# Optimization experiments

Hardware: AMD Instinct MI355X
Metric: run time of the kernel (lower is better)

The kernel has to match this reference:

```python
import jax, jax.numpy as jnp
import numpy as np

B, L, D = 32, 512, 512
H = 512            # d_inner
N_LAYERS = 2
K_SCALE = 1.0
M_SCALE = 1.0
MAX_NORM = 10.0
RMS_EPS = 1e-5


def setup_inputs() -> dict:
    key = jax.random.key(0)
    ks = jax.random.split(key, 12)
    s = 0.02
    x = jax.random.normal(ks[0], (B, L, D), dtype=jnp.float32)
    norm_w = jnp.ones((D,), dtype=jnp.float32)
    W_ih = jax.random.normal(ks[1], (N_LAYERS, D, 2 * H), dtype=jnp.float32) * s
    b_ih = jnp.zeros((N_LAYERS, 2 * H), dtype=jnp.float32)
    W_hh = jax.random.normal(ks[2], (N_LAYERS, H, 2 * H), dtype=jnp.float32) * s
    b_hh = jnp.zeros((N_LAYERS, 2 * H), dtype=jnp.float32)
    # base decay lambdas in [0.01, 0.2] (per KOSLMSSM.__init__), stored as log
    lam = np.linspace(0.01, 0.2, H).astype(np.float32)
    log_lambda = jnp.broadcast_to(jnp.log(jnp.asarray(lam)), (N_LAYERS, H))
    k_W1 = jax.random.normal(ks[3], (N_LAYERS, H, 3 * H), dtype=jnp.float32) * s
    k_b1 = jnp.zeros((N_LAYERS, 3 * H), dtype=jnp.float32)
    k_W2 = jax.random.normal(ks[4], (N_LAYERS, 3 * H, H), dtype=jnp.float32) * s
    k_b2 = jnp.zeros((N_LAYERS, H), dtype=jnp.float32)
    Wo = jax.random.normal(ks[5], (N_LAYERS, H, D), dtype=jnp.float32) * s
    return {"x": x, "norm_w": norm_w, "W_ih": W_ih, "b_ih": b_ih,
            "W_hh": W_hh, "b_hh": b_hh, "log_lambda": log_lambda,
            "k_W1": k_W1, "k_b1": k_b1, "k_W2": k_W2, "k_b2": k_b2, "Wo": Wo}


def _rmsnorm(x, w):
    return x * jax.lax.rsqrt(jnp.mean(x * x, axis=-1, keepdims=True) + RMS_EPS) * w


def _layer(x, norm_w, W_ih, b_ih, W_hh, b_hh, log_lambda, k_W1, k_b1, k_W2, k_b2, Wo):
    xn = _rmsnorm(x, norm_w)
    # input-to-gate projection for the whole sequence (one big GEMM)
    gx = jnp.einsum('bld,dg->blg', xn, W_ih) + b_ih          # [B,L,2H]
    A_base = 1.0 - jnp.exp(log_lambda)                        # [H], stable decay

    def step(carry, g_t):
        h, c, A = carry                                       # each [B,H]
        g = g_t + h @ W_hh + b_hh                             # [B,2H]
        z, m = jnp.split(g, 2, axis=-1)                       # z_raw, m_raw
        M = jnp.tanh(m) * M_SCALE
        innov = z - A * c - M                                 # fused innovation
        kmid = jax.nn.gelu(innov @ k_W1 + k_b1, approximate=False)
        K = jnp.tanh(kmid @ k_W2 + k_b2) * (K_SCALE * 0.5)    # gain
        A_new = A_base * (1.0 - K * K)                        # contractive diag
        c_new = A_new * c + K * innov + M
        sumsq = jnp.sum(c_new * c_new, axis=-1, keepdims=True)
        scale = jnp.minimum(1.0, MAX_NORM * jax.lax.rsqrt(sumsq + 1e-6))
        c_new = c_new * scale
        h_new = c_new
        return (h_new, c_new, A_new), h_new

    z0 = jnp.zeros((x.shape[0], H), dtype=x.dtype)
    _, hs = jax.lax.scan(step, (z0, z0, z0), jnp.swapaxes(gx, 0, 1))
    hs = jnp.swapaxes(hs, 0, 1)                               # [B,L,H]
    return jnp.einsum('blh,hd->bld', hs, Wo)


def reference(x, norm_w, W_ih, b_ih, W_hh, b_hh, log_lambda,
              k_W1, k_b1, k_W2, k_b2, Wo):
    for l in range(N_LAYERS):
        x = _layer(x, norm_w, W_ih[l], b_ih[l], W_hh[l], b_hh[l],
                   log_lambda[l], k_W1[l], k_b1[l], k_W2[l], k_b2[l], Wo[l])
    return x
```

## Files before the change

kernel.cpp:

```cpp
#include <hip/hip_runtime.h>
#include <math.h>

#define BB   32
#define LSEQ 512
#define DD   512
#define HH   512
#define G2H  1024
#define K3H  1536

#define NG   8
#define GWG  64
#define FPAD 16

typedef unsigned int u32;
typedef _Float16 half2_t __attribute__((ext_vector_type(2)));
typedef u32 v4u __attribute__((ext_vector_type(4)));

__device__ __forceinline__ void mload4(v4u& d, const u32* p) {
  asm volatile("global_load_dwordx4 %0, %1, off sc1" : "=v"(d) : "v"(p));
}
__device__ __forceinline__ void vmwait4(v4u& a, v4u& b, v4u& c, v4u& d) {
  asm volatile("s_waitcnt vmcnt(0)"
               : "+v"(a), "+v"(b), "+v"(c), "+v"(d) :: "memory");
}
__device__ __forceinline__ void mstore(u32* p, u32 v) {
  asm volatile("global_store_dword %0, %1, off sc0 sc1" :: "v"(p), "v"(v)
               : "memory");
}

__device__ __forceinline__ float dot2acc(u32 a, u32 b, float acc) {
#if __has_builtin(__builtin_amdgcn_fdot2)
  return __builtin_amdgcn_fdot2(__builtin_bit_cast(half2_t, a),
                                __builtin_bit_cast(half2_t, b), acc, false);
#else
  half2_t ha = __builtin_bit_cast(half2_t, a);
  half2_t hb = __builtin_bit_cast(half2_t, b);
  return acc + (float)ha[0] * (float)hb[0] + (float)ha[1] * (float)hb[1];
#endif
}
__device__ __forceinline__ float dotq(v4u a, v4u b, float acc) {
  acc = dot2acc(a.x, b.x, acc);
  acc = dot2acc(a.y, b.y, acc);
  acc = dot2acc(a.z, b.z, acc);
  acc = dot2acc(a.w, b.w, acc);
  return acc;
}
__device__ __forceinline__ u32 pkf16(float a, float b) {
#if __has_builtin(__builtin_amdgcn_cvt_pkrtz)
  return __builtin_bit_cast(u32, __builtin_amdgcn_cvt_pkrtz(a, b));
#else
  half2_t h; h[0] = (_Float16)a; h[1] = (_Float16)b;
  return __builtin_bit_cast(u32, h);
#endif
}

template<int M> struct TreeC {
  static __device__ __forceinline__ void run(float* a, int lane, int d) {
    const bool hi = (lane & d) != 0;
#pragma unroll
    for (int i = 0; i < M / 2; ++i) {
      float mine  = hi ? a[2 * i + 1] : a[2 * i];
      float yours = hi ? a[2 * i]     : a[2 * i + 1];
      a[i] = mine + __shfl_xor(yours, d, 64);
    }
    TreeC<M / 2>::run(a, lane, d << 1);
  }
};
template<> struct TreeC<1> {
  static __device__ __forceinline__ void run(float*, int, int) {}
};
template<int M>
__device__ __forceinline__ float tree_reduce(float* a, int lane) {
  TreeC<M>::run(a, lane, 1);
  float v = a[0];
#pragma unroll
  for (int d = M; d <= 32; d <<= 1) v += __shfl_xor(v, d, 64);
  return v;
}

__device__ __forceinline__ void xbar(u32* arrive, u32* go, int slot,
                                     unsigned gen, int tid) {
  __syncthreads();
  if (slot == 0) {
    if (tid >= 1 && tid < GWG)
      while (__hip_atomic_load(&arrive[tid * FPAD], __ATOMIC_RELAXED,
                               __HIP_MEMORY_SCOPE_AGENT) < gen) {}
    __syncthreads();
    if (tid == 0) mstore(go, gen);
  } else {
    if (tid == 0) {
      mstore(&arrive[slot * FPAD], gen);
      while (__hip_atomic_load(go, __ATOMIC_RELAXED,
                               __HIP_MEMORY_SCOPE_AGENT) < gen) {}
    }
  }
  __syncthreads();
}

__global__ __launch_bounds__(256)
void rmsnorm_kernel(const float* __restrict__ x, const float* __restrict__ w,
                    float* __restrict__ y)
{
  __shared__ float redl[256];
  const long row = blockIdx.x;
  const int t = threadIdx.x;
  const float* xr = x + row * DD;
  float v0 = xr[t], v1 = xr[t + 256];
  redl[t] = v0 * v0 + v1 * v1;
  __syncthreads();
  for (int off = 128; off > 0; off >>= 1) {
    if (t < off) redl[t] += redl[t + off];
    __syncthreads();
  }
  float scale = rsqrtf(redl[0] * (1.0f / 512.0f) + 1e-5f);
  float* yr = y + row * DD;
  yr[t]       = v0 * scale * w[t];
  yr[t + 256] = v1 * scale * w[t + 256];
}

__global__ __launch_bounds__(256)
void gemm_fp32(const float* __restrict__ A, const float* __restrict__ B,
               const float* __restrict__ bias, float* __restrict__ C,
               int M, int N, int K)
{
  __shared__ float As[16][68];
  __shared__ float Bs[16][64];
  const int t  = threadIdx.x;
  const int tx = t & 15, ty = t >> 4;
  const long m0 = (long)blockIdx.x * 64;
  const long n0 = (long)blockIdx.y * 64;
  const int ar = t >> 2, ac = (t & 3) * 4;
  const int bk = t >> 4, bn = (t & 15) * 4;
  float acc[4][4] = {{0.f}};

  for (int k0 = 0; k0 < K; k0 += 16) {
    float4 av = *(const float4*)(A + (m0 + ar) * K + k0 + ac);
    float4 bv = *(const float4*)(B + (long)(k0 + bk) * N + n0 + bn);
    As[ac + 0][ar] = av.x; As[ac + 1][ar] = av.y;
    As[ac + 2][ar] = av.z; As[ac + 3][ar] = av.w;
    *(float4*)&Bs[bk][bn] = bv;
    __syncthreads();
#pragma unroll
    for (int kk = 0; kk < 16; ++kk) {
      float4 a = *(const float4*)&As[kk][ty * 4];
      float4 b = *(const float4*)&Bs[kk][tx * 4];
      acc[0][0] = fmaf(a.x, b.x, acc[0][0]); acc[0][1] = fmaf(a.x, b.y, acc[0][1]);
      acc[0][2] = fmaf(a.x, b.z, acc[0][2]); acc[0][3] = fmaf(a.x, b.w, acc[0][3]);
      acc[1][0] = fmaf(a.y, b.x, acc[1][0]); acc[1][1] = fmaf(a.y, b.y, acc[1][1]);
      acc[1][2] = fmaf(a.y, b.z, acc[1][2]); acc[1][3] = fmaf(a.y, b.w, acc[1][3]);
      acc[2][0] = fmaf(a.z, b.x, acc[2][0]); acc[2][1] = fmaf(a.z, b.y, acc[2][1]);
      acc[2][2] = fmaf(a.z, b.z, acc[2][2]); acc[2][3] = fmaf(a.z, b.w, acc[2][3]);
      acc[3][0] = fmaf(a.w, b.x, acc[3][0]); acc[3][1] = fmaf(a.w, b.y, acc[3][1]);
      acc[3][2] = fmaf(a.w, b.z, acc[3][2]); acc[3][3] = fmaf(a.w, b.w, acc[3][3]);
    }
    __syncthreads();
  }
  float4 bb = make_float4(0.f, 0.f, 0.f, 0.f);
  if (bias) bb = *(const float4*)(bias + n0 + tx * 4);
#pragma unroll
  for (int i = 0; i < 4; ++i) {
    float4 o;
    o.x = acc[i][0] + bb.x; o.y = acc[i][1] + bb.y;
    o.z = acc[i][2] + bb.z; o.w = acc[i][3] + bb.w;
    *(float4*)(C + (m0 + ty * 4 + i) * N + n0 + tx * 4) = o;
  }
}

__global__ __launch_bounds__(256)
void scan_kernel(const float* __restrict__ gx,
                 const float* __restrict__ Whh, const float* __restrict__ bhh,
                 const float* __restrict__ loglam,
                 const float* __restrict__ kW1, const float* __restrict__ kb1,
                 const float* __restrict__ kW2, const float* __restrict__ kb2,
                 u32* __restrict__ cpk, u32* __restrict__ ipk,
                 u32* __restrict__ kpk, u32* __restrict__ flags,
                 float* __restrict__ hs)
{
  const int blk  = blockIdx.x;
  const int g    = blk & 7;
  const int s    = blk >> 3;
  const int tid  = threadIdx.x;
  const int q    = tid >> 6;
  const int lane = tid & 63;
  const int jz   = s * 8;
  const int jm   = s * 24;

  __shared__ u32 wh[16 * 256];
  __shared__ u32 w1s[24 * 256];
  __shared__ u32 w2s[8 * 768];

  for (int idx = tid; idx < 16 * 256; idx += 256) {
    int c = idx >> 8, p = idx & 255;
    int gcol = (c < 8) ? (jz + c) : (512 + jz + (c - 8));
    wh[idx] = pkf16(Whh[(size_t)(2 * p) * G2H + gcol],
                    Whh[(size_t)(2 * p + 1) * G2H + gcol]);
  }
  for (int idx = tid; idx < 24 * 256; idx += 256) {
    int c = idx >> 8, p = idx & 255;
    w1s[idx] = pkf16(kW1[(size_t)(2 * p) * K3H + jm + c],
                     kW1[(size_t)(2 * p + 1) * K3H + jm + c]);
  }
  for (int idx = tid; idx < 8 * 768; idx += 256) {
    int c = idx / 768, p = idx - c * 768;
    w2s[idx] = pkf16(kW2[(size_t)(2 * p) * HH + jz + c],
                     kW2[(size_t)(2 * p + 1) * HH + jz + c]);
  }

  const int colA = jz + 2 * q + (lane & 1);
  const float Ab   = 1.f - expf(loglam[colA]);
  const float bz   = bhh[colA];
  const float bm   = bhh[512 + colA];
  const float kb2c = kb2[colA];
  int kb1i = lane & 7; if (kb1i > 5) kb1i = 5;
  const float kb1v = kb1[jm + 6 * q + kb1i];

  const int r_st  = (lane >> 1) & 3;
  const int growst = 4 * g + r_st;
  const size_t hsoff = (size_t)growst * LSEQ * HH + colA;
  const size_t gxoff = (size_t)growst * LSEQ * G2H + colA;

  const u32* crow[4]; const u32* irow[4]; const u32* krow[4];
#pragma unroll
  for (int r = 0; r < 4; ++r) {
    crow[r] = cpk + (size_t)(4 * g + r) * 256 + lane * 4;
    irow[r] = ipk + (size_t)(4 * g + r) * 256 + lane * 4;
    krow[r] = kpk + (size_t)(4 * g + r) * 768 + lane * 4;
  }
  u32* arrive = flags + (size_t)g * (GWG + 1) * FPAD;
  u32* goflag = arrive + (size_t)GWG * FPAD;

  if (tid < 16) {
    int r = tid >> 2, j = tid & 3;
    mstore(cpk + (size_t)(4 * g + r) * 256 + 4 * s + j, 0u);
  }
  unsigned gen = 1;
  xbar(arrive, goflag, s, gen, tid);

  float A_own = 0.f, c_own = 0.f, M_own = 0.f, I_own = 0.f, s_own = 1.f;

  for (int it = 0; it <= LSEQ; ++it) {
    float gxz = 0.f, gxm = 0.f;
    if (lane < 8 && it < LSEQ) {
      gxz = gx[gxoff + (size_t)it * G2H];
      gxm = gx[gxoff + (size_t)it * G2H + 512];
    }

    v4u cv0, cv1, cv2, cv3;
    mload4(cv0, crow[0]); mload4(cv1, crow[1]);
    mload4(cv2, crow[2]); mload4(cv3, crow[3]);
    vmwait4(cv0, cv1, cv2, cv3);
    float a4[4] = { dotq(cv0, cv0, 0.f), dotq(cv1, cv1, 0.f),
                    dotq(cv2, cv2, 0.f), dotq(cv3, cv3, 0.f) };
    float a16[16];
#pragma unroll
    for (int t = 0; t < 4; ++t) {
      int col = (t < 2) ? (2 * q + t) : (8 + 2 * q + (t - 2));
      v4u wq = *(const v4u*)(wh + col * 256 + lane * 4);
      a16[0 * 4 + t] = dotq(cv0, wq, 0.f);
      a16[1 * 4 + t] = dotq(cv1, wq, 0.f);
      a16[2 * 4 + t] = dotq(cv2, wq, 0.f);
      a16[3 * 4 + t] = dotq(cv3, wq, 0.f);
    }
    float ssv = tree_reduce<4>(a4, lane);
    float g16 = tree_reduce<16>(a16, lane);
    float sq  = __shfl(ssv, r_st, 64);
    float s_loc = fminf(1.f, 10.f * rsqrtf(sq + 1e-6f));
    float gz = __shfl(g16, (r_st * 4 + (lane & 1)) & 63, 64);
    float gm = __shfl(g16, (r_st * 4 + 2 + (lane & 1)) & 63, 64);
    if (lane < 8 && it >= 1)
      hs[hsoff + (size_t)(it - 1) * HH] = s_loc * c_own;
    if (it == LSEQ) break;
    float gzv = gz * s_loc + gxz + bz;
    float gmv = gm * s_loc + gxm + bm;
    float Mv = tanhf(gmv);
    float iv = gzv - A_own * (s_loc * c_own) - Mv;
    if (lane < 8) { M_own = Mv; I_own = iv; s_own = s_loc; }
    float ivn = __shfl(iv, (lane + 1) & 63, 64);
    if (lane < 8 && !(lane & 1))
      mstore(ipk + (size_t)growst * 256 + 4 * s + q, pkf16(iv, ivn));
    ++gen; xbar(arrive, goflag, s, gen, tid);

    v4u iv0, iv1, iv2, iv3;
    mload4(iv0, irow[0]); mload4(iv1, irow[1]);
    mload4(iv2, irow[2]); mload4(iv3, irow[3]);
    vmwait4(iv0, iv1, iv2, iv3);
    float a32[32];
#pragma unroll
    for (int i = 0; i < 32; ++i) a32[i] = 0.f;
#pragma unroll
    for (int cc = 0; cc < 6; ++cc) {
      v4u wq = *(const v4u*)(w1s + (6 * q + cc) * 256 + lane * 4);
      a32[0 * 8 + cc] = dotq(iv0, wq, 0.f);
      a32[1 * 8 + cc] = dotq(iv1, wq, 0.f);
      a32[2 * 8 + cc] = dotq(iv2, wq, 0.f);
      a32[3 * 8 + cc] = dotq(iv3, wq, 0.f);
    }
    float t32 = tree_reduce<32>(a32, lane);
    float kvb = t32 + kb1v;
    float gl = 0.5f * kvb * (1.f + erff(kvb * 0.7071067811865476f));
    float gln = __shfl(gl, (lane + 1) & 63, 64);
    if (lane < 32 && !(lane & 1) && (lane & 7) < 6) {
      int rr = (lane >> 3) & 3, cc = lane & 7;
      mstore(kpk + (size_t)(4 * g + rr) * 768 + 12 * s + 3 * q + (cc >> 1),
             pkf16(gl, gln));
    }
    ++gen; xbar(arrive, goflag, s, gen, tid);

    v4u k00,k01,k02, k10,k11,k12, k20,k21,k22, k30,k31,k32;
    mload4(k00, krow[0]); mload4(k01, krow[0]+256); mload4(k02, krow[0]+512);
    mload4(k10, krow[1]); mload4(k11, krow[1]+256); mload4(k12, krow[1]+512);
    mload4(k20, krow[2]); mload4(k21, krow[2]+256); mload4(k22, krow[2]+512);
    mload4(k30, krow[3]); mload4(k31, krow[3]+256); mload4(k32, krow[3]+512);
    vmwait4(k00, k01, k02, k10);
    vmwait4(k11, k12, k20, k21);
    vmwait4(k22, k30, k31, k32);
    float a8[8];
#pragma unroll
    for (int ci = 0; ci < 2; ++ci) {
      const u32* wc = w2s + (2 * q + ci) * 768 + lane * 4;
      v4u wq0 = *(const v4u*)(wc);
      v4u wq1 = *(const v4u*)(wc + 256);
      v4u wq2 = *(const v4u*)(wc + 512);
      a8[0 * 2 + ci] = dotq(k02, wq2, dotq(k01, wq1, dotq(k00, wq0, 0.f)));
      a8[1 * 2 + ci] = dotq(k12, wq2, dotq(k11, wq1, dotq(k10, wq0, 0.f)));
      a8[2 * 2 + ci] = dotq(k22, wq2, dotq(k21, wq1, dotq(k20, wq0, 0.f)));
      a8[3 * 2 + ci] = dotq(k32, wq2, dotq(k31, wq1, dotq(k30, wq0, 0.f)));
    }
    float kr = tree_reduce<8>(a8, lane);
    float Kv = tanhf(kr + kb2c) * 0.5f;
    float An = Ab * (1.f - Kv * Kv);
    float cn = An * (s_own * c_own) + Kv * I_own + M_own;
    if (lane < 8) { A_own = An; c_own = cn; }
    float cnn = __shfl(cn, (lane + 1) & 63, 64);
    if (lane < 8 && !(lane & 1))
      mstore(cpk + (size_t)growst * 256 + 4 * s + q, pkf16(cn, cnn));
    ++gen; xbar(arrive, goflag, s, gen, tid);
  }
}

extern "C" void kernel_launch(void* const* d_in, const int* in_sizes, int n_in,
                              void* d_out, int out_size, void* d_ws, size_t ws_size,
                              hipStream_t stream) {
  const float* x      = (const float*)d_in[0];
  const float* norm_w = (const float*)d_in[1];
  const float* W_ih   = (const float*)d_in[2];
  const float* b_ih   = (const float*)d_in[3];
  const float* W_hh   = (const float*)d_in[4];
  const float* b_hh   = (const float*)d_in[5];
  const float* loglam = (const float*)d_in[6];
  const float* kW1    = (const float*)d_in[7];
  const float* kb1    = (const float*)d_in[8];
  const float* kW2    = (const float*)d_in[9];
  const float* kb2    = (const float*)d_in[10];
  const float* Wo     = (const float*)d_in[11];
  float* out = (float*)d_out;

  char* ws = (char*)d_ws;
  float* xn   = (float*)(ws);
  float* gxb  = (float*)(ws + (size_t)33554432);
  float* xmid = (float*)(ws + (size_t)100663296);
  u32* cpk   = (u32*)(ws + (size_t)134217728);
  u32* ipk   = cpk + 8192;
  u32* kpk   = ipk + 8192;
  u32* flags = kpk + 24576;
  float* hs = xn;

  const size_t flag_bytes = (size_t)NG * (GWG + 1) * FPAD * sizeof(u32);

  for (int l = 0; l < 2; ++l) {
    const float* xin = l ? (const float*)xmid : x;
    float* cout = l ? out : xmid;

    rmsnorm_kernel<<<BB * LSEQ, 256, 0, stream>>>(xin, norm_w, xn);

    gemm_fp32<<<dim3(256, 16), 256, 0, stream>>>(
        xn, W_ih + (size_t)l * DD * G2H, b_ih + (size_t)l * G2H, gxb,
        BB * LSEQ, G2H, DD);

    hipMemsetAsync(flags, 0, flag_bytes, stream);
    scan_kernel<<<NG * GWG, 256, 0, stream>>>(
        gxb,
        W_hh + (size_t)l * HH * G2H, b_hh + (size_t)l * G2H,
        loglam + (size_t)l * HH,
        kW1 + (size_t)l * HH * K3H, kb1 + (size_t)l * K3H,
        kW2 + (size_t)l * K3H * HH, kb2 + (size_t)l * HH,
        cpk, ipk, kpk, flags, hs);

    gemm_fp32<<<dim3(256, 8), 256, 0, stream>>>(
        hs, Wo + (size_t)l * HH * DD, nullptr, cout,
        BB * LSEQ, DD, HH);
  }
}
```

Baseline: 10.64 ms.

## Replace centralized grid barrier with per-block tag polling and LDS-staged exchange

Swaps the arrive/go barrier, which had a master block gathering arrivals and then releasing the group, for per-block monotonic tags. Each block publishes its own tag and all 64 lanes poll the group's 64 tags directly, which removes one round trip per phase. Exchanged state is now loaded once per block cooperatively and shared through LDS instead of every wave loading full rows. kW2 moves from shared memory to a pre-packed global buffer read through the cache, freeing LDS. This adds a pack kernel launch, and the global kW2 reads in the inner loop may add latency.

```diff
diff --git a/kernel.cpp b/kernel.cpp
--- a/kernel.cpp
+++ b/kernel.cpp
@@ -10,7 +10,6 @@
 
 #define NG   8
 #define GWG  64
-#define FPAD 16
 
 typedef unsigned int u32;
 typedef _Float16 half2_t __attribute__((ext_vector_type(2)));
@@ -18,10 +17,6 @@
 
 __device__ __forceinline__ void mload4(v4u& d, const u32* p) {
   asm volatile("global_load_dwordx4 %0, %1, off sc1" : "=v"(d) : "v"(p));
-}
-__device__ __forceinline__ void vmwait4(v4u& a, v4u& b, v4u& c, v4u& d) {
-  asm volatile("s_waitcnt vmcnt(0)"
-               : "+v"(a), "+v"(b), "+v"(c), "+v"(d) :: "memory");
 }
 __device__ __forceinline__ void mstore(u32* p, u32 v) {
   asm volatile("global_store_dword %0, %1, off sc0 sc1" :: "v"(p), "v"(v)
@@ -78,22 +73,14 @@
   return v;
 }
 
-__device__ __forceinline__ void xbar(u32* arrive, u32* go, int slot,
-                                     unsigned gen, int tid) {
-  __syncthreads();
-  if (slot == 0) {
-    if (tid >= 1 && tid < GWG)
-      while (__hip_atomic_load(&arrive[tid * FPAD], __ATOMIC_RELAXED,
-                               __HIP_MEMORY_SCOPE_AGENT) < gen) {}
-    __syncthreads();
-    if (tid == 0) mstore(go, gen);
-  } else {
-    if (tid == 0) {
-      mstore(&arrive[slot * FPAD], gen);
-      while (__hip_atomic_load(go, __ATOMIC_RELAXED,
-                               __HIP_MEMORY_SCOPE_AGENT) < gen) {}
-    }
-  }
+__device__ __forceinline__ void poll_tags(const u32* tgg, u32 want, int tid) {
+  const u32* tp = tgg + (tid & 63);
+  while (__hip_atomic_load(tp, __ATOMIC_RELAXED,
+                           __HIP_MEMORY_SCOPE_AGENT) < want) {}
+}
+
+__device__ __forceinline__ void publish_fence() {
+  asm volatile("s_waitcnt vmcnt(0)" ::: "memory");
   __syncthreads();
 }
 
@@ -167,13 +154,23 @@
 }
 
 __global__ __launch_bounds__(256)
+void pack_kw2(const float* __restrict__ kW2, u32* __restrict__ kw2p)
+{
+  int idx = blockIdx.x * 256 + threadIdx.x;
+  int p   = idx % 768;
+  int col = idx / 768;
+  kw2p[idx] = pkf16(kW2[(size_t)(2 * p) * HH + col],
+                    kW2[(size_t)(2 * p + 1) * HH + col]);
+}
+
+__global__ __launch_bounds__(256)
 void scan_kernel(const float* __restrict__ gx,
                  const float* __restrict__ Whh, const float* __restrict__ bhh,
                  const float* __restrict__ loglam,
                  const float* __restrict__ kW1, const float* __restrict__ kb1,
-                 const float* __restrict__ kW2, const float* __restrict__ kb2,
+                 const u32* __restrict__ kw2p, const float* __restrict__ kb2,
                  u32* __restrict__ cpk, u32* __restrict__ ipk,
-                 u32* __restrict__ kpk, u32* __restrict__ flags,
+                 u32* __restrict__ kpk, u32* __restrict__ tags,
                  float* __restrict__ hs)
 {
   const int blk  = blockIdx.x;
@@ -187,7 +184,7 @@
 
   __shared__ u32 wh[16 * 256];
   __shared__ u32 w1s[24 * 256];
-  __shared__ u32 w2s[8 * 768];
+  __shared__ u32 stg[4 * 768];
 
   for (int idx = tid; idx < 16 * 256; idx += 256) {
     int c = idx >> 8, p = idx & 255;
@@ -199,11 +196,6 @@
     int c = idx >> 8, p = idx & 255;
     w1s[idx] = pkf16(kW1[(size_t)(2 * p) * K3H + jm + c],
                      kW1[(size_t)(2 * p + 1) * K3H + jm + c]);
-  }
-  for (int idx = tid; idx < 8 * 768; idx += 256) {
-    int c = idx / 768, p = idx - c * 768;
-    w2s[idx] = pkf16(kW2[(size_t)(2 * p) * HH + jz + c],
-                     kW2[(size_t)(2 * p + 1) * HH + jz + c]);
   }
 
   const int colA = jz + 2 * q + (lane & 1);
@@ -219,36 +211,38 @@
   const size_t hsoff = (size_t)growst * LSEQ * HH + colA;
   const size_t gxoff = (size_t)growst * LSEQ * G2H + colA;
 
-  const u32* crow[4]; const u32* irow[4]; const u32* krow[4];
-#pragma unroll
-  for (int r = 0; r < 4; ++r) {
-    crow[r] = cpk + (size_t)(4 * g + r) * 256 + lane * 4;
-    irow[r] = ipk + (size_t)(4 * g + r) * 256 + lane * 4;
-    krow[r] = kpk + (size_t)(4 * g + r) * 768 + lane * 4;
-  }
-  u32* arrive = flags + (size_t)g * (GWG + 1) * FPAD;
-  u32* goflag = arrive + (size_t)GWG * FPAD;
+  u32* tgg = tags + g * GWG;
 
   if (tid < 16) {
     int r = tid >> 2, j = tid & 3;
     mstore(cpk + (size_t)(4 * g + r) * 256 + 4 * s + j, 0u);
   }
-  unsigned gen = 1;
-  xbar(arrive, goflag, s, gen, tid);
+  publish_fence();
+  if (tid == 0) mstore(tgg + s, 1u);
 
   float A_own = 0.f, c_own = 0.f, M_own = 0.f, I_own = 0.f, s_own = 1.f;
 
   for (int it = 0; it <= LSEQ; ++it) {
+    const u32 base = 3u * (u32)it;
+
     float gxz = 0.f, gxm = 0.f;
     if (lane < 8 && it < LSEQ) {
       gxz = gx[gxoff + (size_t)it * G2H];
       gxm = gx[gxoff + (size_t)it * G2H + 512];
     }
 
-    v4u cv0, cv1, cv2, cv3;
-    mload4(cv0, crow[0]); mload4(cv1, crow[1]);
-    mload4(cv2, crow[2]); mload4(cv3, crow[3]);
-    vmwait4(cv0, cv1, cv2, cv3);
+    poll_tags(tgg, base + 1, tid);
+    {
+      int row = tid >> 6, off = (tid & 63) * 4;
+      v4u t; mload4(t, cpk + (size_t)(4 * g + row) * 256 + off);
+      asm volatile("s_waitcnt vmcnt(0)" ::: "memory");
+      *(v4u*)(stg + row * 256 + off) = t;
+    }
+    __syncthreads();
+    v4u cv0 = *(const v4u*)(stg + 0 * 256 + lane * 4);
+    v4u cv1 = *(const v4u*)(stg + 1 * 256 + lane * 4);
+    v4u cv2 = *(const v4u*)(stg + 2 * 256 + lane * 4);
+    v4u cv3 = *(const v4u*)(stg + 3 * 256 + lane * 4);
     float a4[4] = { dotq(cv0, cv0, 0.f), dotq(cv1, cv1, 0.f),
                     dotq(cv2, cv2, 0.f), dotq(cv3, cv3, 0.f) };
     float a16[16];
@@ -278,12 +272,21 @@
     float ivn = __shfl(iv, (lane + 1) & 63, 64);
     if (lane < 8 && !(lane & 1))
       mstore(ipk + (size_t)growst * 256 + 4 * s + q, pkf16(iv, ivn));
-    ++gen; xbar(arrive, goflag, s, gen, tid);
-
-    v4u iv0, iv1, iv2, iv3;
-    mload4(iv0, irow[0]); mload4(iv1, irow[1]);
-    mload4(iv2, irow[2]); mload4(iv3, irow[3]);
-    vmwait4(iv0, iv1, iv2, iv3);
+    publish_fence();
+    if (tid == 0) mstore(tgg + s, base + 2);
+
+    poll_tags(tgg, base + 2, tid);
+    {
+      int row = tid >> 6, off = (tid & 63) * 4;
+      v4u t; mload4(t, ipk + (size_t)(4 * g + row) * 256 + off);
+      asm volatile("s_waitcnt vmcnt(0)" ::: "memory");
+      *(v4u*)(stg + row * 256 + off) = t;
+    }
+    __syncthreads();
+    v4u iv0 = *(const v4u*)(stg + 0 * 256 + lane * 4);
+    v4u iv1 = *(const v4u*)(stg + 1 * 256 + lane * 4);
+    v4u iv2 = *(const v4u*)(stg + 2 * 256 + lane * 4);
+    v4u iv3 = *(const v4u*)(stg + 3 * 256 + lane * 4);
     float a32[32];
 #pragma unroll
     for (int i = 0; i < 32; ++i) a32[i] = 0.f;
@@ -304,27 +307,38 @@
       mstore(kpk + (size_t)(4 * g + rr) * 768 + 12 * s + 3 * q + (cc >> 1),
              pkf16(gl, gln));
     }
-    ++gen; xbar(arrive, goflag, s, gen, tid);
-
-    v4u k00,k01,k02, k10,k11,k12, k20,k21,k22, k30,k31,k32;
-    mload4(k00, krow[0]); mload4(k01, krow[0]+256); mload4(k02, krow[0]+512);
-    mload4(k10, krow[1]); mload4(k11, krow[1]+256); mload4(k12, krow[1]+512);
-    mload4(k20, krow[2]); mload4(k21, krow[2]+256); mload4(k22, krow[2]+512);
-    mload4(k30, krow[3]); mload4(k31, krow[3]+256); mload4(k32, krow[3]+512);
-    vmwait4(k00, k01, k02, k10);
-    vmwait4(k11, k12, k20, k21);
-    vmwait4(k22, k30, k31, k32);
+    publish_fence();
+    if (tid == 0) mstore(tgg + s, base + 3);
+
+    poll_tags(tgg, base + 3, tid);
+    {
+      int row = tid >> 6, off = (tid & 63) * 4;
+      const u32* src = kpk + (size_t)(4 * g + row) * 768 + off;
+      v4u t0, t1, t2;
+      mload4(t0, src); mload4(t1, src + 256); mload4(t2, src + 512);
+      asm volatile("s_waitcnt vmcnt(0)" ::: "memory");
+      u32* dst = stg + row * 768 + off;
+      *(v4u*)dst = t0; *(v4u*)(dst + 256) = t1; *(v4u*)(dst + 512) = t2;
+    }
+    __syncthreads();
+    v4u kv[4][3];
+#pragma unroll
+    for (int r = 0; r < 4; ++r)
+#pragma unroll
+      for (int j = 0; j < 3; ++j)
+        kv[r][j] = *(const v4u*)(stg + r * 768 + j * 256 + lane * 4);
+    const u32* kw2b = kw2p + (size_t)(8 * s + 2 * q) * 768;
     float a8[8];
 #pragma unroll
     for (int ci = 0; ci < 2; ++ci) {
-      const u32* wc = w2s + (2 * q + ci) * 768 + lane * 4;
-      v4u wq0 = *(const v4u*)(wc);
-      v4u wq1 = *(const v4u*)(wc + 256);
-      v4u wq2 = *(const v4u*)(wc + 512);
-      a8[0 * 2 + ci] = dotq(k02, wq2, dotq(k01, wq1, dotq(k00, wq0, 0.f)));
-      a8[1 * 2 + ci] = dotq(k12, wq2, dotq(k11, wq1, dotq(k10, wq0, 0.f)));
-      a8[2 * 2 + ci] = dotq(k22, wq2, dotq(k21, wq1, dotq(k20, wq0, 0.f)));
-      a8[3 * 2 + ci] = dotq(k32, wq2, dotq(k31, wq1, dotq(k30, wq0, 0.f)));
+      v4u wq0 = *(const v4u*)(kw2b + ci * 768 + 0   + lane * 4);
+      v4u wq1 = *(const v4u*)(kw2b + ci * 768 + 256 + lane * 4);
+      v4u wq2 = *(const v4u*)(kw2b + ci * 768 + 512 + lane * 4);
+#pragma unroll
+      for (int r = 0; r < 4; ++r)
+        a8[r * 2 + ci] = dotq(kv[r][2], wq2,
+                         dotq(kv[r][1], wq1,
+                         dotq(kv[r][0], wq0, 0.f)));
     }
     float kr = tree_reduce<8>(a8, lane);
     float Kv = tanhf(kr + kb2c) * 0.5f;
@@ -334,7 +348,8 @@
     float cnn = __shfl(cn, (lane + 1) & 63, 64);
     if (lane < 8 && !(lane & 1))
       mstore(cpk + (size_t)growst * 256 + 4 * s + q, pkf16(cn, cnn));
-    ++gen; xbar(arrive, goflag, s, gen, tid);
+    publish_fence();
+    if (tid == 0) mstore(tgg + s, base + 4);
   }
 }
 
@@ -359,13 +374,12 @@
   float* xn   = (float*)(ws);
   float* gxb  = (float*)(ws + (size_t)33554432);
   float* xmid = (float*)(ws + (size_t)100663296);
+  u32* kw2p  = (u32*)xmid;
   u32* cpk   = (u32*)(ws + (size_t)134217728);
   u32* ipk   = cpk + 8192;
   u32* kpk   = ipk + 8192;
-  u32* flags = kpk + 24576;
+  u32* tags  = kpk + 24576;
   float* hs = xn;
-
-  const size_t flag_bytes = (size_t)NG * (GWG + 1) * FPAD * sizeof(u32);
 
   for (int l = 0; l < 2; ++l) {
     const float* xin = l ? (const float*)xmid : x;
@@ -377,14 +391,16 @@
         xn, W_ih + (size_t)l * DD * G2H, b_ih + (size_t)l * G2H, gxb,
         BB * LSEQ, G2H, DD);
 
-    hipMemsetAsync(flags, 0, flag_bytes, stream);
+    hipMemsetAsync(tags, 0, NG * GWG * sizeof(u32), stream);
+    pack_kw2<<<1536, 256, 0, stream>>>(kW2 + (size_t)l * K3H * HH, kw2p);
+
     scan_kernel<<<NG * GWG, 256, 0, stream>>>(
         gxb,
         W_hh + (size_t)l * HH * G2H, b_hh + (size_t)l * G2H,
         loglam + (size_t)l * HH,
         kW1 + (size_t)l * HH * K3H, kb1 + (size_t)l * K3H,
-        kW2 + (size_t)l * K3H * HH, kb2 + (size_t)l * HH,
-        cpk, ipk, kpk, flags, hs);
+        kw2p, kb2 + (size_t)l * HH,
+        cpk, ipk, kpk, tags, hs);
 
     gemm_fp32<<<dim3(256, 8), 256, 0, stream>>>(
         hs, Wo + (size_t)l * HH * DD, nullptr, cout,
```

Measured after the change: 33.61 ms. +215.7%, slower.
